# Performance work log

Measured on AMD Instinct MI355X. Metric: run time of the kernel, lower is better.

Reference implementation:

```python
import jax, jax.numpy as jnp
import numpy as np

N = 50000   # nodes
E = 800000  # edges (before self-loops)
IN = 128; H = 4; C = 32; HC = H * C; OUT = 47
EPS = 1e-16  # PyG softmax denominator eps
NEG_SLOPE = 0.2


def setup_inputs() -> dict:
    key = jax.random.key(0)
    ks = jax.random.split(key, 20)
    g = lambda k, shape, s=0.1: (jax.random.normal(k, shape, dtype=jnp.float32) * s)
    inp = {}
    inp["x"] = jax.random.normal(ks[0], (N, IN), dtype=jnp.float32)
    inp["edge_index"] = jax.random.randint(ks[1], (2, E), 0, N, dtype=jnp.int32)
    # layer 0: GATConv(IN -> H*C, concat=True) + skip Linear(IN -> HC)
    inp["lin_w0"] = g(ks[2], (IN, HC)); inp["att_src0"] = g(ks[3], (H, C)); inp["att_dst0"] = g(ks[4], (H, C))
    inp["bias0"] = g(ks[5], (HC,)); inp["skip_w0"] = g(ks[6], (IN, HC)); inp["skip_b0"] = g(ks[7], (HC,))
    # layer 1: GATConv(HC -> H*C, concat=True) + skip Linear(HC -> HC)
    inp["lin_w1"] = g(ks[8], (HC, HC)); inp["att_src1"] = g(ks[9], (H, C)); inp["att_dst1"] = g(ks[10], (H, C))
    inp["bias1"] = g(ks[11], (HC,)); inp["skip_w1"] = g(ks[12], (HC, HC)); inp["skip_b1"] = g(ks[13], (HC,))
    # layer 2: GATConv(HC -> OUT, heads=H, concat=False) + skip Linear(HC -> OUT)
    inp["lin_w2"] = g(ks[14], (HC, H * OUT)); inp["att_src2"] = g(ks[15], (H, OUT)); inp["att_dst2"] = g(ks[16], (H, OUT))
    inp["bias2"] = g(ks[17], (OUT,)); inp["skip_w2"] = g(ks[18], (HC, OUT)); inp["skip_b2"] = g(ks[19], (OUT,))
    return inp


def _gat_conv(x, src, dst, lin_w, att_src, att_dst, bias, concat):
    """PyG GATConv (self-loops already appended to src/dst)."""
    h, c = att_src.shape
    n = x.shape[0]
    xh = (x @ lin_w).reshape(n, h, c)                      # [N, H, C]
    a_src = jnp.einsum('nhc,hc->nh', xh, att_src)          # [N, H]
    a_dst = jnp.einsum('nhc,hc->nh', xh, att_dst)          # [N, H]
    e = a_src[src] + a_dst[dst]                            # [E', H]
    e = jax.nn.leaky_relu(e, NEG_SLOPE)
    # segment softmax over incoming edges per destination node
    m = jax.ops.segment_max(e, dst, num_segments=n)        # [N, H]
    ex = jnp.exp(e - m[dst])
    s = jax.ops.segment_sum(ex, dst, num_segments=n)       # [N, H]
    alpha = ex / (s[dst] + EPS)                            # [E', H]
    out = jax.ops.segment_sum(xh[src] * alpha[:, :, None], dst, num_segments=n)  # [N, H, C]
    out = out.reshape(n, h * c) if concat else out.mean(axis=1)
    return out + bias


def reference(x, edge_index, lin_w0, att_src0, att_dst0, bias0, skip_w0, skip_b0,
              lin_w1, att_src1, att_dst1, bias1, skip_w1, skip_b1,
              lin_w2, att_src2, att_dst2, bias2, skip_w2, skip_b2):
    n = x.shape[0]
    loop = jnp.arange(n, dtype=edge_index.dtype)
    src = jnp.concatenate([edge_index[0], loop])
    dst = jnp.concatenate([edge_index[1], loop])
    # layer 0 (+ skip, ELU; dropout is identity at inference)
    x = _gat_conv(x, src, dst, lin_w0, att_src0, att_dst0, bias0, True) + x @ skip_w0 + skip_b0
    x = jax.nn.elu(x)
    # layer 1
    x = _gat_conv(x, src, dst, lin_w1, att_src1, att_dst1, bias1, True) + x @ skip_w1 + skip_b1
    x = jax.nn.elu(x)
    # layer 2 (concat=False -> head mean), no activation
    x = _gat_conv(x, src, dst, lin_w2, att_src2, att_dst2, bias2, False) + x @ skip_w2 + skip_b2
    return x
```

## Files before the change

### kernel.cpp

```cpp
#include <hip/hip_runtime.h>
#include <math.h>
#include <type_traits>

#define KD 128
#define HC 128
#define NF2 188
#define NF2PB 192
#define OUTC 47

typedef __attribute__((ext_vector_type(8))) __bf16 bf16x8;
typedef __attribute__((ext_vector_type(4))) float f32x4;
typedef __attribute__((ext_vector_type(2))) float f32x2;

#ifdef __has_builtin
#if __has_builtin(__builtin_amdgcn_cvt_pk_f32_fp8)
#define HAVE_CVT_FP8_DEC 1
#endif
#if __has_builtin(__builtin_amdgcn_cvt_pk_fp8_f32)
#define HAVE_CVT_FP8_ENC 1
#endif
#endif

__device__ inline float bfhi_to_f(unsigned int u) {
    union { unsigned int u; float f; } c; c.u = u & 0xFFFF0000u; return c.f;
}
__device__ inline float bflo_to_f(unsigned int u) {
    union { unsigned int u; float f; } c; c.u = u << 16; return c.f;
}
__device__ inline unsigned short f_to_bfu(float f) {
    return __builtin_bit_cast(unsigned short, (__bf16)f);
}
__device__ inline unsigned int pk_bf(float a, float b) {
    return (unsigned int)f_to_bfu(a) | ((unsigned int)f_to_bfu(b) << 16);
}

__device__ inline void dot2bf(float& acc, unsigned int x, unsigned int a) {
    asm("v_dot2_f32_bf16 %0, %1, %2, %0" : "+v"(acc) : "v"(x), "v"(a));
}
__device__ inline unsigned int permb(unsigned int hi, unsigned int lo, unsigned int sel) {
    return __builtin_amdgcn_perm(hi, lo, sel);
}

#ifndef HAVE_CVT_FP8_DEC
__device__ inline float fp8_to_f32_b(unsigned int b) {
    int e = (b >> 3) & 15, m = b & 7;
    float v = e ? ldexpf((float)(8 + m), e - 10) : ldexpf((float)m, -9);
    return (b & 0x80) ? -v : v;
}
#endif
__device__ inline void fp8x4_dec(unsigned int q, float& a, float& b, float& c, float& d) {
#ifdef HAVE_CVT_FP8_DEC
    f32x2 lo = __builtin_amdgcn_cvt_pk_f32_fp8((int)q, false);
    f32x2 hi = __builtin_amdgcn_cvt_pk_f32_fp8((int)q, true);
    a = lo[0]; b = lo[1]; c = hi[0]; d = hi[1];
#else
    a = fp8_to_f32_b(q & 0xFF); b = fp8_to_f32_b((q >> 8) & 0xFF);
    c = fp8_to_f32_b((q >> 16) & 0xFF); d = fp8_to_f32_b((q >> 24) & 0xFF);
#endif
}
__device__ inline unsigned char f32_to_fp8(float v) {
#ifdef HAVE_CVT_FP8_ENC
    return (unsigned char)(__builtin_amdgcn_cvt_pk_fp8_f32(v, v, 0, false) & 0xFF);
#else
    unsigned u = __builtin_bit_cast(unsigned, v);
    unsigned s = (u >> 24) & 0x80;
    float a = fabsf(v);
    if (a < 0.0009765625f) return (unsigned char)s;
    if (a >= 448.f) return (unsigned char)(s | 0x7E);
    int e; float m = frexpf(a, &e);
    int E = e - 1 + 7;
    int mi = (int)rintf(m * 16.f);
    if (mi == 16) { mi = 8; ++E; if (E >= 16) return (unsigned char)(s | 0x7E); }
    if (E <= 0) {
        int q = (int)rintf(a * 512.f); if (q > 7) q = 7;
        return (unsigned char)(s | q);
    }
    return (unsigned char)(s | (E << 3) | (mi - 8));
#endif
}
__device__ inline float fp8dot(unsigned int q, float4 al, float acc) {
    float a, b, c, d;
    fp8x4_dec(q, a, b, c, d);
    return acc + al.x * a + al.y * b + al.z * c + al.w * d;
}

#define NPART 8
#define EPB 2048

__global__ __launch_bounds__(256) void count_kernel(
    const int* __restrict__ dst, int* deg, int e, int rngsz) {
    int r = blockIdx.x & (NPART - 1);
    int chunk = blockIdx.x / NPART;
    int base = chunk * EPB + threadIdx.x * 8;
    int lo = r * rngsz, hi = lo + rngsz;
    if (base >= e) return;
    if (base + 7 < e) {
        int4 d0 = *(const int4*)(dst + base);
        int4 d1 = *(const int4*)(dst + base + 4);
        int dd[8] = {d0.x, d0.y, d0.z, d0.w, d1.x, d1.y, d1.z, d1.w};
#pragma unroll
        for (int k = 0; k < 8; ++k)
            if (dd[k] >= lo && dd[k] < hi) atomicAdd(&deg[dd[k]], 1);
    } else {
        for (int k = base; k < e; ++k) {
            int d = dst[k];
            if (d >= lo && d < hi) atomicAdd(&deg[d], 1);
        }
    }
}

__global__ __launch_bounds__(256) void scan_base_kernel(
    int* __restrict__ deg, int* counter,
    int* __restrict__ row_ptr, int* __restrict__ fill, int* __restrict__ col, int n) {
    int i = blockIdx.x * 256 + threadIdx.x;
    int v = (i < n) ? (deg[i] + 1) : 0;
    int lane = threadIdx.x & 63, w = threadIdx.x >> 6;
    int incl = v;
#pragma unroll
    for (int off = 1; off < 64; off <<= 1) {
        int u = __shfl_up(incl, off, 64);
        if (lane >= off) incl += u;
    }
    __shared__ int wsum[4];
    __shared__ int base_sh;
    if (lane == 63) wsum[w] = incl;
    __syncthreads();
    if (threadIdx.x == 0)
        base_sh = atomicAdd(counter, wsum[0] + wsum[1] + wsum[2] + wsum[3]);
    int woff = 0;
    for (int k = 0; k < w; ++k) woff += wsum[k];
    __syncthreads();
    int excl = base_sh + woff + incl - v;
    if (i < n) {
        row_ptr[i] = excl;
        col[excl] = i;
        fill[i] = excl + 1;
        deg[i] = v;
    }
}

__global__ __launch_bounds__(256) void fill_kernel(
    const int* __restrict__ ei, int* fill, int* col, int e, int rngsz) {
    int r = blockIdx.x & (NPART - 1);
    int chunk = blockIdx.x / NPART;
    int base = chunk * EPB + threadIdx.x * 8;
    int lo = r * rngsz, hi = lo + rngsz;
    if (base >= e) return;
    const int* dstp = ei + e;
    if (base + 7 < e) {
        int4 d0 = *(const int4*)(dstp + base);
        int4 d1 = *(const int4*)(dstp + base + 4);
        int dd[8] = {d0.x, d0.y, d0.z, d0.w, d1.x, d1.y, d1.z, d1.w};
#pragma unroll
        for (int k = 0; k < 8; ++k) {
            if (dd[k] >= lo && dd[k] < hi) {
                int pos = atomicAdd(&fill[dd[k]], 1);
                col[pos] = ei[base + k];
            }
        }
    } else {
        for (int k = base; k < e; ++k) {
            int d = dstp[k];
            if (d >= lo && d < hi) {
                int pos = atomicAdd(&fill[d], 1);
                col[pos] = ei[k];
            }
        }
    }
}

__global__ __launch_bounds__(256) void prep_w_kernel(
    const float* __restrict__ lw0, const float* __restrict__ sw0,
    const float* __restrict__ lw1, const float* __restrict__ sw1,
    const float* __restrict__ lw2, const float* __restrict__ sw2,
    __bf16* __restrict__ bt) {
    int idx = blockIdx.x * 256 + threadIdx.x;
    int buf = idx >> 15;
    int r = idx & 32767;
    int n = r >> 7, k = r & 127;
    float v = 0.f;
    if (buf == 0) v = (n < 128) ? lw0[k * 128 + n] : sw0[k * 128 + n - 128];
    else if (buf == 1) v = (n < 128) ? lw1[k * 128 + n] : sw1[k * 128 + n - 128];
    else {
        if (n < 188) v = lw2[k * 188 + n];
        else if (n >= 192 && n < 239) v = sw2[k * 47 + n - 192];
    }
    bt[idx] = (__bf16)v;
}

template <typename AT, typename SKT, int NLIN, int NSK, int TR>
__global__ __launch_bounds__(256) void gemm_fused_kernel(
    const AT* __restrict__ A, const __bf16* __restrict__ Bt,
    void* __restrict__ out0, int N0, int ldc0,
    const float* __restrict__ bias1, SKT* __restrict__ out1, int N1, int M) {
    __shared__ __bf16 As[64][136];
    __shared__ __bf16 Bs[64][136];
    int tid = threadIdx.x;
    int m0 = blockIdx.x * 64;

#pragma unroll
    for (int rep = 0; rep < 4; ++rep) {
        int idx = tid + rep * 256;
        int row = idx >> 4, seg = idx & 15;
        int gm = m0 + row;
        bf16x8 v = {};
        if (gm < M) {
            if constexpr (std::is_same<AT, float>::value) {
                const float* p = A + gm * KD + seg * 8;
                float4 f0 = *(const float4*)p;
                float4 f1 = *(const float4*)(p + 4);
                v[0] = (__bf16)f0.x; v[1] = (__bf16)f0.y; v[2] = (__bf16)f0.z; v[3] = (__bf16)f0.w;
                v[4] = (__bf16)f1.x; v[5] = (__bf16)f1.y; v[6] = (__bf16)f1.z; v[7] = (__bf16)f1.w;
            } else {
                v = *(const bf16x8*)(A + gm * KD + seg * 8);
            }
        }
        *(bf16x8*)&As[row][seg * 8] = v;
    }
    __syncthreads();

    int w = tid >> 6, lane = tid & 63;
    int lr = lane & 15, quad = lane >> 4;

#pragma unroll
    for (int t = 0; t < NLIN + NSK; ++t) {
        bool second = t >= NLIN;
        int N = second ? N1 : N0;
        int n0 = (second ? (t - NLIN) : t) * 64;
        if (t) __syncthreads();
#pragma unroll
        for (int rep = 0; rep < 4; ++rep) {
            int idx = tid + rep * 256;
            int row = idx >> 4, seg = idx & 15;
            *(bf16x8*)&Bs[row][seg * 8] =
                *(const bf16x8*)(Bt + ((t * 64 + row) << 7) + seg * 8);
        }
        __syncthreads();

        f32x4 acc[4] = {};
#pragma unroll
        for (int kc = 0; kc < 128; kc += 32) {
            bf16x8 a0 = *(const bf16x8*)&As[w * 16 + lr][kc + quad * 8];
            bf16x8 b0 = *(const bf16x8*)&Bs[lr][kc + quad * 8];
            bf16x8 b1 = *(const bf16x8*)&Bs[16 + lr][kc + quad * 8];
            bf16x8 b2 = *(const bf16x8*)&Bs[32 + lr][kc + quad * 8];
            bf16x8 b3 = *(const bf16x8*)&Bs[48 + lr][kc + quad * 8];
            acc[0] = __builtin_amdgcn_mfma_f32_16x16x32_bf16(a0, b0, acc[0], 0, 0, 0);
            acc[1] = __builtin_amdgcn_mfma_f32_16x16x32_bf16(a0, b1, acc[1], 0, 0, 0);
            acc[2] = __builtin_amdgcn_mfma_f32_16x16x32_bf16(a0, b2, acc[2], 0, 0, 0);
            acc[3] = __builtin_amdgcn_mfma_f32_16x16x32_bf16(a0, b3, acc[3], 0, 0, 0);
        }
#pragma unroll
        for (int c = 0; c < 4; ++c) {
#pragma unroll
            for (int reg = 0; reg < 4; ++reg) {
                int row = m0 + w * 16 + quad * 4 + reg;
                int colg = n0 + c * 16 + lr;
                if (row < M && colg < N) {
                    float v = acc[c][reg];
                    if (second) {
                        v += bias1[colg];
                        out1[row * N + colg] = (SKT)v;
                    } else if (TR) {
                        int h = (colg * 1395) >> 16;
                        ((unsigned char*)out0)[row * ldc0 + (colg - 47 * h) * 4 + h] =
                            f32_to_fp8(v);
                    } else {
                        ((__bf16*)out0)[((colg >> 5) * M + row) * 32 + (colg & 31)] =
                            (__bf16)v;
                    }
                }
            }
        }
    }
}

__global__ __launch_bounds__(256) void att_kernel(
    const uint4* __restrict__ xh, const float* __restrict__ att_s,
    const float* __restrict__ att_d, float* __restrict__ a_src,
    float* __restrict__ a_dst, int n) {
    int tid = blockIdx.x * 256 + threadIdx.x;
    int node = tid >> 4;
    int l16 = threadIdx.x & 15;
    if (node >= n) return;
    int p = l16 >> 2, sub = l16 & 3;
    uint4 q = xh[((size_t)p * n + node) * 4 + sub];
    int f0 = l16 * 8;
    float4 as0 = *(const float4*)(att_s + f0);
    float4 as1 = *(const float4*)(att_s + f0 + 4);
    float4 ad0 = *(const float4*)(att_d + f0);
    float4 ad1 = *(const float4*)(att_d + f0 + 4);
    float x0 = bflo_to_f(q.x), x1 = bfhi_to_f(q.x);
    float x2 = bflo_to_f(q.y), x3 = bfhi_to_f(q.y);
    float x4 = bflo_to_f(q.z), x5 = bfhi_to_f(q.z);
    float x6 = bflo_to_f(q.w), x7 = bfhi_to_f(q.w);
    float hs = x0 * as0.x + x1 * as0.y + x2 * as0.z + x3 * as0.w
             + x4 * as1.x + x5 * as1.y + x6 * as1.z + x7 * as1.w;
    float hd = x0 * ad0.x + x1 * ad0.y + x2 * ad0.z + x3 * ad0.w
             + x4 * ad1.x + x5 * ad1.y + x6 * ad1.z + x7 * ad1.w;
    hs += __shfl_xor(hs, 1, 64); hs += __shfl_xor(hs, 2, 64);
    hd += __shfl_xor(hd, 1, 64); hd += __shfl_xor(hd, 2, 64);
    if ((l16 & 3) == 0) {
        int h = l16 >> 2;
        a_src[node * 4 + h] = hs;
        a_dst[node * 4 + h] = hd;
    }
}

__global__ __launch_bounds__(256) void att2_kernel(
    const unsigned char* __restrict__ xh8, const float* __restrict__ att_s,
    const float* __restrict__ att_d, float* __restrict__ a_src,
    float* __restrict__ a_dst, int n) {
    int node = (blockIdx.x * 256 + threadIdx.x) >> 6;
    int lane = threadIdx.x & 63;
    if (node >= n) return;
    float ps0 = 0.f, ps1 = 0.f, ps2 = 0.f, ps3 = 0.f;
    float pd0 = 0.f, pd1 = 0.f, pd2 = 0.f, pd3 = 0.f;
    if (lane < 47) {
        unsigned int q = ((const unsigned int*)(xh8 + node * NF2PB))[lane];
        float x0, x1, x2, x3;
        fp8x4_dec(q, x0, x1, x2, x3);
        ps0 = x0 * att_s[lane];       ps1 = x1 * att_s[47 + lane];
        ps2 = x2 * att_s[94 + lane];  ps3 = x3 * att_s[141 + lane];
        pd0 = x0 * att_d[lane];       pd1 = x1 * att_d[47 + lane];
        pd2 = x2 * att_d[94 + lane];  pd3 = x3 * att_d[141 + lane];
    }
#pragma unroll
    for (int off = 1; off <= 32; off <<= 1) {
        ps0 += __shfl_xor(ps0, off, 64); ps1 += __shfl_xor(ps1, off, 64);
        ps2 += __shfl_xor(ps2, off, 64); ps3 += __shfl_xor(ps3, off, 64);
        pd0 += __shfl_xor(pd0, off, 64); pd1 += __shfl_xor(pd1, off, 64);
        pd2 += __shfl_xor(pd2, off, 64); pd3 += __shfl_xor(pd3, off, 64);
    }
    if (lane < 4) {
        float vs = (lane == 0) ? ps0 : (lane == 1) ? ps1 : (lane == 2) ? ps2 : ps3;
        float vd = (lane == 0) ? pd0 : (lane == 1) ? pd1 : (lane == 2) ? pd2 : pd3;
        a_src[node * 4 + lane] = vs;
        a_dst[node * 4 + lane] = vd;
    }
}

__global__ __launch_bounds__(256) void alpha2_kernel(
    const float* __restrict__ a_src, const float* __restrict__ a_dst,
    const int* __restrict__ row_ptr, const int* __restrict__ deg,
    const int* __restrict__ col, unsigned short* __restrict__ alp,
    int epad, int n) {
    int grp = threadIdx.x >> 4;
    int l16 = threadIdx.x & 15;
    int node = (blockIdx.x << 4) + grp;
    bool active = node < n;
    int node_c = active ? node : 0;
    int start = row_ptr[node_c];
    int end = start + (active ? deg[node_c] : 0);
    float4 ad4 = *(const float4*)(a_dst + 4 * node_c);

    float s0 = 0.f, s1 = 0.f, s2 = 0.f, s3 = 0.f;
    float e00 = 0.f, e01 = 0.f, e02 = 0.f, e03 = 0.f;
    float e10 = 0.f, e11 = 0.f, e12 = 0.f, e13 = 0.f;
    int c = 0;
    for (int base = start; base < end; base += 16, ++c) {
        int e = base + l16;
        bool ok = e < end;
        int j = ok ? col[e] : 0;
        float4 as4 = *(const float4*)(a_src + 4 * j);
        float v0 = as4.x + ad4.x; v0 = v0 > 0.f ? v0 : 0.2f * v0;
        float v1 = as4.y + ad4.y; v1 = v1 > 0.f ? v1 : 0.2f * v1;
        float v2 = as4.z + ad4.z; v2 = v2 > 0.f ? v2 : 0.2f * v2;
        float v3 = as4.w + ad4.w; v3 = v3 > 0.f ? v3 : 0.2f * v3;
        float x0 = ok ? __expf(v0) : 0.f;
        float x1 = ok ? __expf(v1) : 0.f;
        float x2 = ok ? __expf(v2) : 0.f;
        float x3 = ok ? __expf(v3) : 0.f;
        s0 += x0; s1 += x1; s2 += x2; s3 += x3;
        if (c == 0) { e00 = x0; e01 = x1; e02 = x2; e03 = x3; }
        else if (c == 1) { e10 = x0; e11 = x1; e12 = x2; e13 = x3; }
    }
#pragma unroll
    for (int off = 1; off <= 8; off <<= 1) {
        s0 += __shfl_xor(s0, off, 64);
        s1 += __shfl_xor(s1, off, 64);
        s2 += __shfl_xor(s2, off, 64);
        s3 += __shfl_xor(s3, off, 64);
    }
    float i0 = 1.f / (s0 + 1e-16f), i1 = 1.f / (s1 + 1e-16f);
    float i2 = 1.f / (s2 + 1e-16f), i3 = 1.f / (s3 + 1e-16f);

    c = 0;
    for (int base = start; base < end; base += 16, ++c) {
        float al0, al1, al2, al3;
        if (c == 0) {
            al0 = e00 * i0; al1 = e01 * i1; al2 = e02 * i2; al3 = e03 * i3;
        } else if (c == 1) {
            al0 = e10 * i0; al1 = e11 * i1; al2 = e12 * i2; al3 = e13 * i3;
        } else {
            int e = base + l16;
            bool ok = e < end;
            int j = ok ? col[e] : 0;
            float4 as4 = *(const float4*)(a_src + 4 * j);
            float v0 = as4.x + ad4.x; v0 = v0 > 0.f ? v0 : 0.2f * v0;
            float v1 = as4.y + ad4.y; v1 = v1 > 0.f ? v1 : 0.2f * v1;
            float v2 = as4.z + ad4.z; v2 = v2 > 0.f ? v2 : 0.2f * v2;
            float v3 = as4.w + ad4.w; v3 = v3 > 0.f ? v3 : 0.2f * v3;
            al0 = ok ? __expf(v0) * i0 : 0.f;
            al1 = ok ? __expf(v1) * i1 : 0.f;
            al2 = ok ? __expf(v2) * i2 : 0.f;
            al3 = ok ? __expf(v3) * i3 : 0.f;
        }
        int e = base + l16;
        if (active && e < end) {
            alp[e]            = f_to_bfu(al0);
            alp[epad + e]     = f_to_bfu(al1);
            alp[2 * epad + e] = f_to_bfu(al2);
            alp[3 * epad + e] = f_to_bfu(al3);
        }
    }
}

__global__ __launch_bounds__(256) void gather2_kernel(
    const uint4* __restrict__ xh, const unsigned short* __restrict__ alp,
    int epad, const uint4* __restrict__ skipb, const float* __restrict__ bias,
    const int* __restrict__ row_ptr, const int* __restrict__ deg,
    const int* __restrict__ col, uint4* __restrict__ outp, int n) {
    int q = blockIdx.x & 3;
    int nb = blockIdx.x >> 2;
    int node = nb * 64 + (threadIdx.x >> 2);
    if (node >= n) return;
    int l4 = threadIdx.x & 3;
    int s = row_ptr[node];
    int cnt = deg[node];
    int end = s + cnt;
    int k0 = s >> 1, kend = (end - 1) >> 1;
    unsigned m0 = (s & 1) ? 0xFFFF0000u : 0xFFFFFFFFu;
    unsigned mL = (end & 1) ? 0x0000FFFFu : 0xFFFFFFFFu;
    const unsigned* alq = (const unsigned*)(alp + (size_t)q * epad);
    const uint4* xq = xh + (size_t)q * n * 4;

    float a0 = 0.f, a1 = 0.f, a2 = 0.f, a3 = 0.f;
    float a4 = 0.f, a5 = 0.f, a6 = 0.f, a7 = 0.f;
    for (int k = k0; k <= kend; ++k) {
        unsigned au = alq[k];
        if (k == k0) au &= m0;
        if (k == kend) au &= mL;
        int2 jj = *(const int2*)(col + 2 * k);
        uint4 qa = xq[jj.x * 4 + l4];
        uint4 qb = xq[jj.y * 4 + l4];
        dot2bf(a0, permb(qb.x, qa.x, 0x05040100u), au);
        dot2bf(a1, permb(qb.x, qa.x, 0x07060302u), au);
        dot2bf(a2, permb(qb.y, qa.y, 0x05040100u), au);
        dot2bf(a3, permb(qb.y, qa.y, 0x07060302u), au);
        dot2bf(a4, permb(qb.z, qa.z, 0x05040100u), au);
        dot2bf(a5, permb(qb.z, qa.z, 0x07060302u), au);
        dot2bf(a6, permb(qb.w, qa.w, 0x05040100u), au);
        dot2bf(a7, permb(qb.w, qa.w, 0x07060302u), au);
    }

    int xoff = q * 4 + l4;
    int f = q * 32 + l4 * 8;
    float4 b0 = *(const float4*)(bias + f);
    float4 b1 = *(const float4*)(bias + f + 4);
    uint4 skq = skipb[node * 16 + xoff];
    float v0 = a0 + b0.x + bflo_to_f(skq.x);
    float v1 = a1 + b0.y + bfhi_to_f(skq.x);
    float v2 = a2 + b0.z + bflo_to_f(skq.y);
    float v3 = a3 + b0.w + bfhi_to_f(skq.y);
    float v4 = a4 + b1.x + bflo_to_f(skq.z);
    float v5 = a5 + b1.y + bfhi_to_f(skq.z);
    float v6 = a6 + b1.z + bflo_to_f(skq.w);
    float v7 = a7 + b1.w + bfhi_to_f(skq.w);
    v0 = v0 > 0.f ? v0 : (__expf(v0) - 1.f);
    v1 = v1 > 0.f ? v1 : (__expf(v1) - 1.f);
    v2 = v2 > 0.f ? v2 : (__expf(v2) - 1.f);
    v3 = v3 > 0.f ? v3 : (__expf(v3) - 1.f);
    v4 = v4 > 0.f ? v4 : (__expf(v4) - 1.f);
    v5 = v5 > 0.f ? v5 : (__expf(v5) - 1.f);
    v6 = v6 > 0.f ? v6 : (__expf(v6) - 1.f);
    v7 = v7 > 0.f ? v7 : (__expf(v7) - 1.f);
    outp[node * 16 + xoff] =
        make_uint4(pk_bf(v0, v1), pk_bf(v2, v3), pk_bf(v4, v5), pk_bf(v6, v7));
}

__global__ __launch_bounds__(256) void agg1_kernel(
    const unsigned int* __restrict__ x8, const float* __restrict__ a_src,
    const float* __restrict__ a_dst, const float* __restrict__ skip,
    const float* __restrict__ bias, const int* __restrict__ row_ptr,
    const int* __restrict__ deg, const int* __restrict__ col,
    float* __restrict__ outp, int n) {
    __shared__ float s_af[4][64][4];
    __shared__ int s_j[4][64];
    int w = threadIdx.x >> 6;
    int lane = threadIdx.x & 63;
    int node = (blockIdx.x << 2) + w;
    bool active = node < n;
    int node_c = active ? node : 0;
    int start = row_ptr[node_c];
    int end = start + (active ? deg[node_c] : 0);
    float4 ad4 = *(const float4*)(a_dst + 4 * node_c);
    float adh[4] = {ad4.x, ad4.y, ad4.z, ad4.w};

    int e0 = start + lane;
    bool ok0 = e0 < end;
    int jcap = ok0 ? col[e0] : 0;
    float evc[4];
    {
        float4 as4 = *(const float4*)(a_src + 4 * jcap);
        float v0 = as4.x + adh[0]; v0 = v0 > 0.f ? v0 : 0.2f * v0;
        float v1 = as4.y + adh[1]; v1 = v1 > 0.f ? v1 : 0.2f * v1;
        float v2 = as4.z + adh[2]; v2 = v2 > 0.f ? v2 : 0.2f * v2;
        float v3 = as4.w + adh[3]; v3 = v3 > 0.f ? v3 : 0.2f * v3;
        evc[0] = ok0 ? __expf(v0) : 0.f;
        evc[1] = ok0 ? __expf(v1) : 0.f;
        evc[2] = ok0 ? __expf(v2) : 0.f;
        evc[3] = ok0 ? __expf(v3) : 0.f;
    }
    float s[4] = {evc[0], evc[1], evc[2], evc[3]};
    for (int e = e0 + 64; e < end; e += 64) {
        int j = col[e];
        float4 as4 = *(const float4*)(a_src + 4 * j);
        float ev[4] = {as4.x + adh[0], as4.y + adh[1], as4.z + adh[2], as4.w + adh[3]};
#pragma unroll
        for (int h = 0; h < 4; ++h) {
            float v = ev[h] > 0.f ? ev[h] : 0.2f * ev[h];
            s[h] += __expf(v);
        }
    }
#pragma unroll
    for (int off = 32; off >= 1; off >>= 1)
#pragma unroll
        for (int h = 0; h < 4; ++h) s[h] += __shfl_xor(s[h], off, 64);
    float inv[4];
#pragma unroll
    for (int h = 0; h < 4; ++h) inv[h] = 1.f / (s[h] + 1e-16f);

    bool lv = lane < 47;
    float acc0 = 0.f;

    auto run_chunk = [&](int cnt) {
        int t = 0;
        for (; t + 7 < cnt; t += 8) {
            unsigned int q0 = lv ? x8[s_j[w][t] * 48 + lane] : 0u;
            unsigned int q1 = lv ? x8[s_j[w][t + 1] * 48 + lane] : 0u;
            unsigned int q2 = lv ? x8[s_j[w][t + 2] * 48 + lane] : 0u;
            unsigned int q3 = lv ? x8[s_j[w][t + 3] * 48 + lane] : 0u;
            unsigned int q4 = lv ? x8[s_j[w][t + 4] * 48 + lane] : 0u;
            unsigned int q5 = lv ? x8[s_j[w][t + 5] * 48 + lane] : 0u;
            unsigned int q6 = lv ? x8[s_j[w][t + 6] * 48 + lane] : 0u;
            unsigned int q7 = lv ? x8[s_j[w][t + 7] * 48 + lane] : 0u;
            acc0 = fp8dot(q0, *(const float4*)&s_af[w][t][0], acc0);
            acc0 = fp8dot(q1, *(const float4*)&s_af[w][t + 1][0], acc0);
            acc0 = fp8dot(q2, *(const float4*)&s_af[w][t + 2][0], acc0);
            acc0 = fp8dot(q3, *(const float4*)&s_af[w][t + 3][0], acc0);
            acc0 = fp8dot(q4, *(const float4*)&s_af[w][t + 4][0], acc0);
            acc0 = fp8dot(q5, *(const float4*)&s_af[w][t + 5][0], acc0);
            acc0 = fp8dot(q6, *(const float4*)&s_af[w][t + 6][0], acc0);
            acc0 = fp8dot(q7, *(const float4*)&s_af[w][t + 7][0], acc0);
        }
        for (; t + 3 < cnt; t += 4) {
            unsigned int q0 = lv ? x8[s_j[w][t] * 48 + lane] : 0u;
            unsigned int q1 = lv ? x8[s_j[w][t + 1] * 48 + lane] : 0u;
            unsigned int q2 = lv ? x8[s_j[w][t + 2] * 48 + lane] : 0u;
            unsigned int q3 = lv ? x8[s_j[w][t + 3] * 48 + lane] : 0u;
            acc0 = fp8dot(q0, *(const float4*)&s_af[w][t][0], acc0);
            acc0 = fp8dot(q1, *(const float4*)&s_af[w][t + 1][0], acc0);
            acc0 = fp8dot(q2, *(const float4*)&s_af[w][t + 2][0], acc0);
            acc0 = fp8dot(q3, *(const float4*)&s_af[w][t + 3][0], acc0);
        }
        for (; t < cnt; ++t) {
            unsigned int q = lv ? x8[s_j[w][t] * 48 + lane] : 0u;
            acc0 = fp8dot(q, *(const float4*)&s_af[w][t][0], acc0);
        }
    };

    {
        float al[4];
#pragma unroll
        for (int h = 0; h < 4; ++h) al[h] = evc[h] * inv[h];
        s_j[w][lane] = jcap;
        *(float4*)&s_af[w][lane][0] = make_float4(al[0], al[1], al[2], al[3]);
        int cnt = end - start; if (cnt > 64) cnt = 64;
        run_chunk(cnt);
    }
    for (int base = start + 64; base < end; base += 64) {
        int e = base + lane;
        bool ok = e < end;
        int jv = ok ? col[e] : 0;
        float4 as4 = *(const float4*)(a_src + 4 * jv);
        float al[4];
#pragma unroll
        for (int h = 0; h < 4; ++h) {
            float ev = ((const float*)&as4)[h] + adh[h];
            ev = ev > 0.f ? ev : 0.2f * ev;
            al[h] = ok ? __expf(ev) * inv[h] : 0.f;
        }
        s_j[w][lane] = jv;
        *(float4*)&s_af[w][lane][0] = make_float4(al[0], al[1], al[2], al[3]);
        int cnt = end - base; if (cnt > 64) cnt = 64;
        run_chunk(cnt);
    }

    if (active && lane < OUTC) {
        float v = acc0 * 0.25f + bias[lane] + skip[node * OUTC + lane];
        outp[node * OUTC + lane] = v;
    }
}

extern "C" void kernel_launch(void* const* d_in, const int* in_sizes, int n_in,
                              void* d_out, int out_size, void* d_ws, size_t ws_size,
                              hipStream_t stream) {
    const float* x        = (const float*)d_in[0];
    const int*   ei       = (const int*)d_in[1];
    const float* lin_w0   = (const float*)d_in[2];
    const float* att_src0 = (const float*)d_in[3];
    const float* att_dst0 = (const float*)d_in[4];
    const float* bias0    = (const float*)d_in[5];
    const float* skip_w0  = (const float*)d_in[6];
    const float* skip_b0  = (const float*)d_in[7];
    const float* lin_w1   = (const float*)d_in[8];
    const float* att_src1 = (const float*)d_in[9];
    const float* att_dst1 = (const float*)d_in[10];
    const float* bias1    = (const float*)d_in[11];
    const float* skip_w1  = (const float*)d_in[12];
    const float* skip_b1  = (const float*)d_in[13];
    const float* lin_w2   = (const float*)d_in[14];
    const float* att_src2 = (const float*)d_in[15];
    const float* att_dst2 = (const float*)d_in[16];
    const float* bias2    = (const float*)d_in[17];
    const float* skip_w2  = (const float*)d_in[18];
    const float* skip_b2  = (const float*)d_in[19];
    float* out = (float*)d_out;

    const int N = in_sizes[0] / KD;
    const int E = in_sizes[1] / 2;
    const int ET_ = E + N;

    char* ws = (char*)d_ws;
    size_t off = 0;
    auto alloc = [&](size_t bytes) -> void* {
        void* p = ws + off;
        off = (off + bytes + 255) & ~(size_t)255;
        return p;
    };
    void*   xh      = alloc((size_t)N * HC * 2 + 256);
    __bf16* buf_bf  = (__bf16*)alloc((size_t)N * HC * 2);
    void*   skipbuf = alloc((size_t)N * HC * 2);
    float* a_src    = (float*)alloc((size_t)N * 4 * 4);
    float* a_dst    = (float*)alloc((size_t)N * 4 * 4);
    int* deg        = (int*)alloc((size_t)N * 4);
    int* row_ptr    = (int*)alloc((size_t)N * 4);
    int* fill       = (int*)alloc((size_t)N * 4);
    int* col        = (int*)alloc((size_t)(ET_ + 16) * 4);
    int* counter    = (int*)alloc(256);
    __bf16* Bt      = (__bf16*)alloc((size_t)3 * 256 * 128 * 2);
    int epad        = (ET_ + 64) & ~63;
    unsigned short* alp = (unsigned short*)alloc((size_t)4 * epad * 2);

    prep_w_kernel<<<384, 256, 0, stream>>>(lin_w0, skip_w0, lin_w1, skip_w1,
                                           lin_w2, skip_w2, Bt);

    hipMemsetAsync(deg, 0, (size_t)N * 4, stream);
    hipMemsetAsync(counter, 0, 4, stream);
    hipMemsetAsync(col + ET_, 0, 64, stream);
    int rngsz = (N + NPART - 1) / NPART;
    int cblocks = ((E + EPB - 1) / EPB) * NPART;
    count_kernel<<<cblocks, 256, 0, stream>>>(ei + E, deg, E, rngsz);
    scan_base_kernel<<<(N + 255) / 256, 256, 0, stream>>>(deg, counter, row_ptr, fill, col, N);
    fill_kernel<<<cblocks, 256, 0, stream>>>(ei, fill, col, E, rngsz);

    dim3 blk(256);
    int mblocks = (N + 63) / 64;
    int wave_blocks = (N + 3) / 4;
    int a_blocks = (N + 15) / 16;
    int g_blocks = ((N + 63) / 64) * 4;
    int att_blocks = (N * 16 + 255) / 256;

    gemm_fused_kernel<float, __bf16, 2, 2, 0><<<mblocks, blk, 0, stream>>>(
        x, Bt, xh, HC, HC, skip_b0, (__bf16*)skipbuf, HC, N);
    att_kernel<<<att_blocks, blk, 0, stream>>>((const uint4*)xh, att_src0, att_dst0,
                                               a_src, a_dst, N);
    alpha2_kernel<<<a_blocks, blk, 0, stream>>>(a_src, a_dst, row_ptr, deg, col,
                                                alp, epad, N);
    gather2_kernel<<<g_blocks, blk, 0, stream>>>((const uint4*)xh, alp, epad,
                                                 (const uint4*)skipbuf, bias0,
                                                 row_ptr, deg, col,
                                                 (uint4*)buf_bf, N);
    gemm_fused_kernel<__bf16, __bf16, 2, 2, 0><<<mblocks, blk, 0, stream>>>(
        buf_bf, Bt + 32768, xh, HC, HC, skip_b1, (__bf16*)skipbuf, HC, N);
    att_kernel<<<att_blocks, blk, 0, stream>>>((const uint4*)xh, att_src1, att_dst1,
                                               a_src, a_dst, N);
    alpha2_kernel<<<a_blocks, blk, 0, stream>>>(a_src, a_dst, row_ptr, deg, col,
                                                alp, epad, N);
    gather2_kernel<<<g_blocks, blk, 0, stream>>>((const uint4*)xh, alp, epad,
                                                 (const uint4*)skipbuf, bias1,
                                                 row_ptr, deg, col,
                                                 (uint4*)buf_bf, N);
    gemm_fused_kernel<__bf16, float, 3, 1, 1><<<mblocks, blk, 0, stream>>>(
        buf_bf, Bt + 65536, xh, NF2, NF2PB, skip_b2, (float*)skipbuf, OUTC, N);
    att2_kernel<<<wave_blocks, blk, 0, stream>>>((const unsigned char*)xh, att_src2,
                                                 att_dst2, a_src, a_dst, N);
    agg1_kernel<<<wave_blocks, blk, 0, stream>>>((const unsigned int*)xh, a_src, a_dst,
                                                 (const float*)skipbuf, bias2,
                                                 row_ptr, deg, col, out, N);
}
```

Baseline: 419.5 us.

## Fuse edge softmax into per-head gather kernel, dropping alpha buffer

```diff
diff --git a/kernel.cpp b/kernel.cpp
--- a/kernel.cpp
+++ b/kernel.cpp
@@ -340,87 +340,12 @@
     }
 }
 
-__global__ __launch_bounds__(256) void alpha2_kernel(
-    const float* __restrict__ a_src, const float* __restrict__ a_dst,
-    const int* __restrict__ row_ptr, const int* __restrict__ deg,
-    const int* __restrict__ col, unsigned short* __restrict__ alp,
-    int epad, int n) {
-    int grp = threadIdx.x >> 4;
-    int l16 = threadIdx.x & 15;
-    int node = (blockIdx.x << 4) + grp;
-    bool active = node < n;
-    int node_c = active ? node : 0;
-    int start = row_ptr[node_c];
-    int end = start + (active ? deg[node_c] : 0);
-    float4 ad4 = *(const float4*)(a_dst + 4 * node_c);
-
-    float s0 = 0.f, s1 = 0.f, s2 = 0.f, s3 = 0.f;
-    float e00 = 0.f, e01 = 0.f, e02 = 0.f, e03 = 0.f;
-    float e10 = 0.f, e11 = 0.f, e12 = 0.f, e13 = 0.f;
-    int c = 0;
-    for (int base = start; base < end; base += 16, ++c) {
-        int e = base + l16;
-        bool ok = e < end;
-        int j = ok ? col[e] : 0;
-        float4 as4 = *(const float4*)(a_src + 4 * j);
-        float v0 = as4.x + ad4.x; v0 = v0 > 0.f ? v0 : 0.2f * v0;
-        float v1 = as4.y + ad4.y; v1 = v1 > 0.f ? v1 : 0.2f * v1;
-        float v2 = as4.z + ad4.z; v2 = v2 > 0.f ? v2 : 0.2f * v2;
-        float v3 = as4.w + ad4.w; v3 = v3 > 0.f ? v3 : 0.2f * v3;
-        float x0 = ok ? __expf(v0) : 0.f;
-        float x1 = ok ? __expf(v1) : 0.f;
-        float x2 = ok ? __expf(v2) : 0.f;
-        float x3 = ok ? __expf(v3) : 0.f;
-        s0 += x0; s1 += x1; s2 += x2; s3 += x3;
-        if (c == 0) { e00 = x0; e01 = x1; e02 = x2; e03 = x3; }
-        else if (c == 1) { e10 = x0; e11 = x1; e12 = x2; e13 = x3; }
-    }
-#pragma unroll
-    for (int off = 1; off <= 8; off <<= 1) {
-        s0 += __shfl_xor(s0, off, 64);
-        s1 += __shfl_xor(s1, off, 64);
-        s2 += __shfl_xor(s2, off, 64);
-        s3 += __shfl_xor(s3, off, 64);
-    }
-    float i0 = 1.f / (s0 + 1e-16f), i1 = 1.f / (s1 + 1e-16f);
-    float i2 = 1.f / (s2 + 1e-16f), i3 = 1.f / (s3 + 1e-16f);
-
-    c = 0;
-    for (int base = start; base < end; base += 16, ++c) {
-        float al0, al1, al2, al3;
-        if (c == 0) {
-            al0 = e00 * i0; al1 = e01 * i1; al2 = e02 * i2; al3 = e03 * i3;
-        } else if (c == 1) {
-            al0 = e10 * i0; al1 = e11 * i1; al2 = e12 * i2; al3 = e13 * i3;
-        } else {
-            int e = base + l16;
-            bool ok = e < end;
-            int j = ok ? col[e] : 0;
-            float4 as4 = *(const float4*)(a_src + 4 * j);
-            float v0 = as4.x + ad4.x; v0 = v0 > 0.f ? v0 : 0.2f * v0;
-            float v1 = as4.y + ad4.y; v1 = v1 > 0.f ? v1 : 0.2f * v1;
-            float v2 = as4.z + ad4.z; v2 = v2 > 0.f ? v2 : 0.2f * v2;
-            float v3 = as4.w + ad4.w; v3 = v3 > 0.f ? v3 : 0.2f * v3;
-            al0 = ok ? __expf(v0) * i0 : 0.f;
-            al1 = ok ? __expf(v1) * i1 : 0.f;
-            al2 = ok ? __expf(v2) * i2 : 0.f;
-            al3 = ok ? __expf(v3) * i3 : 0.f;
-        }
-        int e = base + l16;
-        if (active && e < end) {
-            alp[e]            = f_to_bfu(al0);
-            alp[epad + e]     = f_to_bfu(al1);
-            alp[2 * epad + e] = f_to_bfu(al2);
-            alp[3 * epad + e] = f_to_bfu(al3);
-        }
-    }
-}
-
-__global__ __launch_bounds__(256) void gather2_kernel(
-    const uint4* __restrict__ xh, const unsigned short* __restrict__ alp,
-    int epad, const uint4* __restrict__ skipb, const float* __restrict__ bias,
-    const int* __restrict__ row_ptr, const int* __restrict__ deg,
-    const int* __restrict__ col, uint4* __restrict__ outp, int n) {
+__global__ __launch_bounds__(256) void agg0q_kernel(
+    const uint4* __restrict__ xh, const float* __restrict__ a_src,
+    const float* __restrict__ a_dst, const uint4* __restrict__ skipb,
+    const float* __restrict__ bias, const int* __restrict__ row_ptr,
+    const int* __restrict__ deg, const int* __restrict__ col,
+    uint4* __restrict__ outp, int n) {
     int q = blockIdx.x & 3;
     int nb = blockIdx.x >> 2;
     int node = nb * 64 + (threadIdx.x >> 2);
@@ -429,19 +354,33 @@
     int s = row_ptr[node];
     int cnt = deg[node];
     int end = s + cnt;
+    float ad = a_dst[4 * node + q];
+
+    float ssum = 0.f;
+    for (int e = s + l4; e < end; e += 4) {
+        int j = col[e];
+        float v = a_src[4 * j + q] + ad;
+        v = v > 0.f ? v : 0.2f * v;
+        ssum += __expf(v);
+    }
+    ssum += __shfl_xor(ssum, 1, 64);
+    ssum += __shfl_xor(ssum, 2, 64);
+    float inv = 1.f / (ssum + 1e-16f);
+
     int k0 = s >> 1, kend = (end - 1) >> 1;
     unsigned m0 = (s & 1) ? 0xFFFF0000u : 0xFFFFFFFFu;
     unsigned mL = (end & 1) ? 0x0000FFFFu : 0xFFFFFFFFu;
-    const unsigned* alq = (const unsigned*)(alp + (size_t)q * epad);
     const uint4* xq = xh + (size_t)q * n * 4;
 
     float a0 = 0.f, a1 = 0.f, a2 = 0.f, a3 = 0.f;
     float a4 = 0.f, a5 = 0.f, a6 = 0.f, a7 = 0.f;
     for (int k = k0; k <= kend; ++k) {
-        unsigned au = alq[k];
+        int2 jj = *(const int2*)(col + 2 * k);
+        float vl = a_src[4 * jj.x + q] + ad; vl = vl > 0.f ? vl : 0.2f * vl;
+        float vh = a_src[4 * jj.y + q] + ad; vh = vh > 0.f ? vh : 0.2f * vh;
+        unsigned au = pk_bf(__expf(vl) * inv, __expf(vh) * inv);
         if (k == k0) au &= m0;
         if (k == kend) au &= mL;
-        int2 jj = *(const int2*)(col + 2 * k);
         uint4 qa = xq[jj.x * 4 + l4];
         uint4 qb = xq[jj.y * 4 + l4];
         dot2bf(a0, permb(qb.x, qa.x, 0x05040100u), au);
@@ -650,8 +589,6 @@
     int* col        = (int*)alloc((size_t)(ET_ + 16) * 4);
     int* counter    = (int*)alloc(256);
     __bf16* Bt      = (__bf16*)alloc((size_t)3 * 256 * 128 * 2);
-    int epad        = (ET_ + 64) & ~63;
-    unsigned short* alp = (unsigned short*)alloc((size_t)4 * epad * 2);
 
     prep_w_kernel<<<384, 256, 0, stream>>>(lin_w0, skip_w0, lin_w1, skip_w1,
                                            lin_w2, skip_w2, Bt);
@@ -668,7 +605,6 @@
     dim3 blk(256);
     int mblocks = (N + 63) / 64;
     int wave_blocks = (N + 3) / 4;
-    int a_blocks = (N + 15) / 16;
     int g_blocks = ((N + 63) / 64) * 4;
     int att_blocks = (N * 16 + 255) / 256;
 
@@ -676,22 +612,18 @@
         x, Bt, xh, HC, HC, skip_b0, (__bf16*)skipbuf, HC, N);
     att_kernel<<<att_blocks, blk, 0, stream>>>((const uint4*)xh, att_src0, att_dst0,
                                                a_src, a_dst, N);
-    alpha2_kernel<<<a_blocks, blk, 0, stream>>>(a_src, a_dst, row_ptr, deg, col,
-                                                alp, epad, N);
-    gather2_kernel<<<g_blocks, blk, 0, stream>>>((const uint4*)xh, alp, epad,
-                                                 (const uint4*)skipbuf, bias0,
-                                                 row_ptr, deg, col,
-                                                 (uint4*)buf_bf, N);
+    agg0q_kernel<<<g_blocks, blk, 0, stream>>>((const uint4*)xh, a_src, a_dst,
+                                               (const uint4*)skipbuf, bias0,
+                                               row_ptr, deg, col,
+                                               (uint4*)buf_bf, N);
     gemm_fused_kernel<__bf16, __bf16, 2, 2, 0><<<mblocks, blk, 0, stream>>>(
         buf_bf, Bt + 32768, xh, HC, HC, skip_b1, (__bf16*)skipbuf, HC, N);
     att_kernel<<<att_blocks, blk, 0, stream>>>((const uint4*)xh, att_src1, att_dst1,
                                                a_src, a_dst, N);
-    alpha2_kernel<<<a_blocks, blk, 0, stream>>>(a_src, a_dst, row_ptr, deg, col,
-                                                alp, epad, N);
-    gather2_kernel<<<g_blocks, blk, 0, stream>>>((const uint4*)xh, alp, epad,
-                                                 (const uint4*)skipbuf, bias1,
-                                                 row_ptr, deg, col,
-                                                 (uint4*)buf_bf, N);
+    agg0q_kernel<<<g_blocks, blk, 0, stream>>>((const uint4*)xh, a_src, a_dst,
+                                               (const uint4*)skipbuf, bias1,
+                                               row_ptr, deg, col,
+                                               (uint4*)buf_bf, N);
     gemm_fused_kernel<__bf16, float, 3, 1, 1><<<mblocks, blk, 0, stream>>>(
         buf_bf, Bt + 65536, xh, NF2, NF2PB, skip_b2, (float*)skipbuf, OUTC, N);
     att2_kernel<<<wave_blocks, blk, 0, stream>>>((const unsigned char*)xh, att_src2,
```

Result: slower. 456.7 us (+8.9%).
